# Kernel optimization log

Hardware: AMD Instinct MI355X
Metric: run time of the kernel (lower is better)

## Reference

```python
import jax, jax.numpy as jnp
import numpy as np

HEADS = 16


def setup_inputs() -> dict:
    key = jax.random.key(0)
    ks = jax.random.split(key, 7)
    B, N, MEM, DIM = 2, 2048, 2048, 1024
    J = MEM + N
    x = jax.random.normal(ks[0], (B, N, DIM), dtype=jnp.float32)
    mem = jax.random.normal(ks[1], (B, MEM, DIM), dtype=jnp.float32)
    expire_mask = jax.random.uniform(ks[2], (B, 1, 1, J), dtype=jnp.float32)
    Wq = jax.random.normal(ks[3], (DIM, DIM), dtype=jnp.float32) * 0.02
    Wkv = jax.random.normal(ks[4], (DIM, 2 * DIM), dtype=jnp.float32) * 0.02
    Wo = jax.random.normal(ks[5], (DIM, DIM), dtype=jnp.float32) * 0.02
    bo = jnp.zeros((DIM,), dtype=jnp.float32)
    return {"x": x, "mem": mem, "expire_mask": expire_mask,
            "Wq": Wq, "Wkv": Wkv, "Wo": Wo, "bo": bo}


def reference(x, mem, expire_mask, Wq, Wkv, Wo, bo):
    b, n, dim = x.shape
    h = HEADS
    d = dim // h
    scale = d ** -0.5
    mem_len = mem.shape[1]

    q = x @ Wq                                   # [b, n, dim]
    context = jnp.concatenate([mem, x], axis=1)  # [b, j, dim]
    kv = context @ Wkv                           # [b, j, 2*dim]
    k, v = jnp.split(kv, 2, axis=-1)

    def to_heads(t):
        bb, nn, _ = t.shape
        return t.reshape(bb, nn, h, d).transpose(0, 2, 1, 3)  # b h n d

    q, k, v = map(to_heads, (q, k, v))

    dots = jnp.einsum('bhid,bhjd->bhij', q, k) * scale  # [b,h,n,j]
    j_len = dots.shape[-1]
    # causal mask with memory offset: position i attends to j <= i + mem_len
    i_idx = jnp.arange(n)[:, None]
    j_idx = jnp.arange(j_len)[None, :]
    causal = j_idx > (i_idx + mem_len)           # True => masked
    dots = jnp.where(causal[None, None], -jnp.inf, dots)

    attn = jax.nn.softmax(dots, axis=-1)
    attn = attn * expire_mask                    # post-softmax expire gating

    out = jnp.einsum('bhij,bhjd->bhid', attn, v)  # [b,h,n,d]
    out = out.transpose(0, 2, 1, 3).reshape(b, n, dim)
    return out @ Wo + bo
```

## Files before the change

### kernel.cpp

```cpp
#include <hip/hip_runtime.h>
#include <cstdint>

typedef __bf16 bf16_t;
typedef __attribute__((ext_vector_type(2))) __bf16 bf16x2;
typedef __attribute__((ext_vector_type(4))) __bf16 bf16x4;
typedef __attribute__((ext_vector_type(8))) __bf16 bf16x8;
typedef __attribute__((ext_vector_type(4))) float f32x4;
typedef __attribute__((ext_vector_type(16))) float f32x16;
typedef __attribute__((ext_vector_type(4))) int i32x4;

constexpr int Bx = 2, Nx = 2048, MEMx = 2048, Jx = 4096, DIMx = 1024, Hx = 16, HDx = 64;

__device__ __forceinline__ void gload_lds16(const bf16_t* g, bf16_t* lds) {
  __builtin_amdgcn_global_load_lds(
      (const __attribute__((address_space(1))) unsigned int*)g,
      (__attribute__((address_space(3))) unsigned int*)lds, 16, 0, 0);
}

__device__ __forceinline__ int pk2(float a, float b) {
  bf16x2 t;
  t[0] = (bf16_t)a;
  t[1] = (bf16_t)b;
  return __builtin_bit_cast(int, t);
}

__device__ __forceinline__ void pl32swap(int& a, int& b) {
  asm volatile("v_permlane32_swap_b32 %0, %1" : "+v"(a), "+v"(b));
}

__device__ __forceinline__ float fmax3(float a, float b, float c) {
  float d;
  asm("v_max3_f32 %0, %1, %2, %3" : "=v"(d) : "v"(a), "v"(b), "v"(c));
  return d;
}

__global__ void k_build_bf16(const float* __restrict__ x, const float* __restrict__ mem,
                             bf16_t* __restrict__ xb, bf16_t* __restrict__ ctxb) {
  const int XT = Bx * Nx * DIMx;
  const int CT = Bx * Jx * DIMx;
  for (int i = blockIdx.x * blockDim.x + threadIdx.x; i < XT + CT;
       i += gridDim.x * blockDim.x) {
    if (i < XT) {
      xb[i] = (bf16_t)x[i];
    } else {
      int c = i - XT;
      int bb = c / (Jx * DIMx);
      int rr = c % (Jx * DIMx);
      int j = rr / DIMx, d = rr % DIMx;
      float v = (j < MEMx) ? mem[(int64_t)(bb * MEMx + j) * DIMx + d]
                           : x[(int64_t)(bb * Nx + (j - MEMx)) * DIMx + d];
      ctxb[c] = (bf16_t)v;
    }
  }
}

__global__ void k_transpose_w(const float* __restrict__ W, bf16_t* __restrict__ WT,
                              int K, int Nc) {
  int total = K * Nc;
  for (int i = blockIdx.x * blockDim.x + threadIdx.x; i < total;
       i += gridDim.x * blockDim.x) {
    int n = i / K, k = i % K;
    WT[i] = (bf16_t)W[(int64_t)k * Nc + n];
  }
}

template <int MODE>
__launch_bounds__(256)
__global__ void k_gemm_bt(const bf16_t* __restrict__ A, const bf16_t* __restrict__ BT,
                          void* __restrict__ Cv, const float* __restrict__ bias,
                          const float* __restrict__ gate, bf16_t* __restrict__ VT,
                          float scale, int M, int Nc, int K) {
  __shared__ bf16_t As[2][128 * 32];
  __shared__ bf16_t Bs[2][128 * 32];
  const int tid = threadIdx.x;
  const int w = tid >> 6, l = tid & 63;
  const int lr = l & 15, lg = l >> 4;
  const int m0 = blockIdx.y * 128, n0 = blockIdx.x * 128;
  const int wm = (w >> 1) * 64, wn = (w & 1) * 64;

  const int srow = w * 16 + (l >> 2);
  const int scol = (l & 3) * 8;
  const bf16_t* ga0 = A + (int64_t)(m0 + srow) * K + scol;
  const bf16_t* gb0 = BT + (int64_t)(n0 + srow) * K + scol;

  auto stage = [&](int bufi, int k0) {
    bf16_t* lA = &As[bufi][0] + w * 512;
    bf16_t* lB = &Bs[bufi][0] + w * 512;
    gload_lds16(ga0 + k0, lA);
    gload_lds16(ga0 + (int64_t)64 * K + k0, lA + 2048);
    gload_lds16(gb0 + k0, lB);
    gload_lds16(gb0 + (int64_t)64 * K + k0, lB + 2048);
  };

  f32x4 acc[4][4] = {};

  stage(0, 0);
  __syncthreads();

  const int nsteps = K >> 5;
  for (int t = 0; t < nsteps; ++t) {
    const int cur = t & 1;
    if (t + 1 < nsteps) stage(cur ^ 1, (t + 1) << 5);

    bf16x8 af[4], bfr[4];
#pragma unroll
    for (int q = 0; q < 4; ++q)
      af[q] = *(const bf16x8*)(&As[cur][0] + (wm + q * 16 + lr) * 32 + lg * 8);
#pragma unroll
    for (int q = 0; q < 4; ++q)
      bfr[q] = *(const bf16x8*)(&Bs[cur][0] + (wn + q * 16 + lr) * 32 + lg * 8);
#pragma unroll
    for (int mt = 0; mt < 4; ++mt)
#pragma unroll
      for (int nt = 0; nt < 4; ++nt)
        acc[mt][nt] = __builtin_amdgcn_mfma_f32_16x16x32_bf16(af[mt], bfr[nt],
                                                              acc[mt][nt], 0, 0, 0);
    __syncthreads();
  }

#pragma unroll
  for (int mt = 0; mt < 4; ++mt) {
#pragma unroll
    for (int nt = 0; nt < 4; ++nt) {
      int col = n0 + wn + nt * 16 + lr;
      int row0 = m0 + wm + mt * 16 + lg * 4;
      if constexpr (MODE == 0) {
#pragma unroll
        for (int r = 0; r < 4; ++r)
          ((bf16_t*)Cv)[(int64_t)(row0 + r) * Nc + col] =
              (bf16_t)(acc[mt][nt][r] * scale);
      } else if constexpr (MODE == 1) {
#pragma unroll
        for (int r = 0; r < 4; ++r)
          ((float*)Cv)[(int64_t)(row0 + r) * Nc + col] = acc[mt][nt][r] + bias[col];
      } else {
        if (col < 1024) {
#pragma unroll
          for (int r = 0; r < 4; ++r)
            ((bf16_t*)Cv)[(int64_t)(row0 + r) * 1024 + col] = (bf16_t)acc[mt][nt][r];
        } else {
          int hh = (col - 1024) >> 6, dd = col & 63;
          int bb = row0 >> 12, jj = row0 & (Jx - 1);
          bf16x4 ov;
#pragma unroll
          for (int r = 0; r < 4; ++r)
            ov[r] = (bf16_t)(acc[mt][nt][r] * gate[row0 + r]);
          *(bf16x4*)(VT + (((int64_t)(bb * Hx + hh) * HDx + dd) << 12) + jj) = ov;
        }
      }
    }
  }
}

__launch_bounds__(256)
__global__ void k_attn(const bf16_t* __restrict__ Q, const bf16_t* __restrict__ Kbuf,
                       const bf16_t* __restrict__ VT, bf16_t* __restrict__ Opart,
                       float2* __restrict__ ML) {
  __shared__ bf16_t Ks[2][64 * 64];
  __shared__ bf16_t Vs[2][64 * 64];

  const int tid = threadIdx.x;
  const int w = tid >> 6, l = tid & 63;
  const int ql = l & 31, hi = l >> 5;

  const int lin = blockIdx.x;
  const int qi0 = lin & 15, h = (lin >> 4) & 15;
  const int c = (lin >> 8) & 1, b = lin >> 9;
  const int qi = b ? (15 - qi0) : qi0;
  const int q0 = qi * 128;

  const bf16_t* Qb = Q + ((int64_t)b * Nx) * DIMx + h * HDx;
  const bf16_t* Kb = Kbuf + ((int64_t)b * Jx) * 1024 + h * HDx;
  const bf16_t* Vb = VT + ((int64_t)(b * Hx + h) * HDx << 12);

  const int qrow = q0 + w * 32 + ql;

  bf16x8 qf[4];
#pragma unroll
  for (int dt = 0; dt < 4; ++dt)
    qf[dt] = *(const bf16x8*)(Qb + (int64_t)qrow * DIMx + dt * 16 + hi * 8);
  asm volatile("s_waitcnt vmcnt(0)" ::: "memory");

  int koff[2][4], voff[2][4];
#pragma unroll
  for (int jb = 0; jb < 2; ++jb)
#pragma unroll
    for (int dt = 0; dt < 4; ++dt)
      koff[jb][dt] = (jb * 32 + ql) * 128 + (((dt * 2 + hi) * 16) ^ ((ql & 7) * 16));
#pragma unroll
  for (int db = 0; db < 2; ++db)
#pragma unroll
    for (int jt = 0; jt < 4; ++jt)
      voff[db][jt] = (db * 32 + ql) * 128 + (((jt * 2 + hi) * 16) ^ ((ql & 7) * 16));

  f32x16 o[2] = {};
  float mrun = -1e30f, lsum = 0.f;

  const int srow8 = l >> 3;
  const int swcol = ((l & 7) ^ srow8) * 8;
  const int jstart = c * 2048;
  const int jend = c ? ((Jx < q0 + 128 + MEMx) ? Jx : (q0 + 128 + MEMx)) : 2048;
  const int nt_tiles = (jend - jstart) >> 6;
  const f32x16 z16 = {};

  const bf16_t* ksrc0 = Kb + (int64_t)(w * 16 + srow8) * 1024 + swcol;
  const bf16_t* vsrc0 = Vb + (int64_t)(w * 16 + srow8) * Jx + swcol;

  auto stage = [&](int bufi, int j0) {
    bf16_t* kd = &Ks[bufi][0] + w * 1024;
    const bf16_t* ks = ksrc0 + (int64_t)j0 * 1024;
    gload_lds16(ks, kd);
    gload_lds16(ks + 8 * 1024, kd + 512);
    bf16_t* vd = &Vs[bufi][0] + w * 1024;
    const bf16_t* vs = vsrc0 + j0;
    gload_lds16(vs, vd);
    gload_lds16(vs + 8 * Jx, vd + 512);
  };

  stage(0, jstart);
  stage(1, jstart + 64);

  for (int t = 0; t < nt_tiles; ++t) {
    const int cur = t & 1;
    const int j0 = jstart + (t << 6);
    if (t + 1 < nt_tiles)
      asm volatile("s_waitcnt vmcnt(4)" ::: "memory");
    else
      asm volatile("s_waitcnt vmcnt(0)" ::: "memory");
    __builtin_amdgcn_s_barrier();
    __builtin_amdgcn_sched_barrier(0);

    const char* KsC = (const char*)&Ks[cur][0];
    const char* VsC = (const char*)&Vs[cur][0];

    f32x16 s[2];
    __builtin_amdgcn_s_setprio(1);
#pragma unroll
    for (int jb = 0; jb < 2; ++jb) {
      f32x16 acc = z16;
#pragma unroll
      for (int dt = 0; dt < 4; ++dt) {
        bf16x8 kf = *(const bf16x8*)(KsC + koff[jb][dt]);
        acc = __builtin_amdgcn_mfma_f32_32x32x16_bf16(kf, qf[dt], acc, 0, 0, 0);
      }
      s[jb] = acc;
    }
    __builtin_amdgcn_s_setprio(0);

    if (j0 + 63 > q0 + MEMx) {
#pragma unroll
      for (int jb = 0; jb < 2; ++jb)
#pragma unroll
        for (int r = 0; r < 16; ++r) {
          int j = j0 + jb * 32 + (r & 3) + (r >> 2) * 8 + hi * 4;
          if (j > qrow + MEMx) s[jb][r] = -1e30f;
        }
    }

    float t12[12];
#pragma unroll
    for (int i = 0; i < 10; ++i)
      t12[i] = fmax3(s[(3 * i) >> 4][(3 * i) & 15], s[(3 * i + 1) >> 4][(3 * i + 1) & 15],
                     s[(3 * i + 2) >> 4][(3 * i + 2) & 15]);
    t12[10] = s[1][14];
    t12[11] = s[1][15];
    float t4[4];
#pragma unroll
    for (int i = 0; i < 4; ++i) t4[i] = fmax3(t12[3 * i], t12[3 * i + 1], t12[3 * i + 2]);
    float tm = fmaxf(fmax3(t4[0], t4[1], t4[2]), t4[3]);
    tm = fmaxf(tm, __shfl_xor(tm, 32));

    if (!__all(tm <= mrun + 8.f)) {
      float mnew = fmaxf(mrun, tm);
      float al = exp2f(mrun - mnew);
      mrun = mnew;
      lsum *= al;
#pragma unroll
      for (int db = 0; db < 2; ++db)
#pragma unroll
        for (int r = 0; r < 16; ++r) o[db][r] *= al;
    }

#pragma unroll
    for (int jb = 0; jb < 2; ++jb)
#pragma unroll
      for (int r = 0; r < 16; ++r) s[jb][r] = exp2f(s[jb][r] - mrun);

    f32x16 av = s[0] + s[1];
    float a8[8], a4[4];
#pragma unroll
    for (int i = 0; i < 8; ++i) a8[i] = av[i] + av[i + 8];
#pragma unroll
    for (int i = 0; i < 4; ++i) a4[i] = a8[i] + a8[i + 4];
    float ps = (a4[0] + a4[1]) + (a4[2] + a4[3]);
    ps += __shfl_xor(ps, 32);
    lsum += ps;

    bf16x8 pfrag[4];
#pragma unroll
    for (int jb = 0; jb < 2; ++jb) {
      int pw[8];
#pragma unroll
      for (int g = 0; g < 8; ++g) pw[g] = pk2(s[jb][2 * g], s[jb][2 * g + 1]);
      pl32swap(pw[0], pw[2]);
      pl32swap(pw[1], pw[3]);
      pl32swap(pw[4], pw[6]);
      pl32swap(pw[5], pw[7]);
      i32x4 f0 = {pw[0], pw[1], pw[2], pw[3]};
      i32x4 f1 = {pw[4], pw[5], pw[6], pw[7]};
      pfrag[jb * 2] = __builtin_bit_cast(bf16x8, f0);
      pfrag[jb * 2 + 1] = __builtin_bit_cast(bf16x8, f1);
    }

    __builtin_amdgcn_s_setprio(1);
#pragma unroll
    for (int db = 0; db < 2; ++db)
#pragma unroll
      for (int jt = 0; jt < 4; ++jt) {
        bf16x8 vf = *(const bf16x8*)(VsC + voff[db][jt]);
        o[db] = __builtin_amdgcn_mfma_f32_32x32x16_bf16(vf, pfrag[jt], o[db], 0, 0, 0);
      }
    __builtin_amdgcn_s_setprio(0);

    __builtin_amdgcn_s_barrier();
    __builtin_amdgcn_sched_barrier(0);
    if (t + 2 < nt_tiles) stage(cur, jstart + ((t + 2) << 6));
  }

  bf16_t* op = Opart + (int64_t)c * (Bx * Nx * DIMx) +
               (int64_t)(b * Nx + qrow) * DIMx + h * HDx;
#pragma unroll
  for (int db = 0; db < 2; ++db)
#pragma unroll
    for (int g = 0; g < 4; ++g) {
      bf16x4 ov;
#pragma unroll
      for (int r = 0; r < 4; ++r) ov[r] = (bf16_t)o[db][g * 4 + r];
      *(bf16x4*)(op + db * 32 + g * 8 + hi * 4) = ov;
    }
  if (hi == 0)
    ML[((int64_t)(c * Bx + b) * Hx + h) * Nx + qrow] = make_float2(mrun, lsum);
}

__global__ void k_combine(const bf16_t* __restrict__ Op, const float2* __restrict__ ML,
                          bf16_t* __restrict__ Ho) {
  const int64_t CH = (int64_t)Bx * Nx * DIMx;
  int i = blockIdx.x * blockDim.x + threadIdx.x;
  const int total = (int)(CH >> 3);
  if (i >= total) return;
  int64_t off = (int64_t)i * 8;
  int bqh = (int)(off >> 6);
  int h = bqh & 15;
  int bq = bqh >> 4;
  int b = bq >> 11, q = bq & (Nx - 1);
  float2 ml0 = ML[((int64_t)b * Hx + h) * Nx + q];
  float2 ml1 = ML[((int64_t)(Bx + b) * Hx + h) * Nx + q];
  float M = fmaxf(ml0.x, ml1.x);
  float a0 = exp2f(ml0.x - M), a1 = exp2f(ml1.x - M);
  float inv = 1.f / (a0 * ml0.y + a1 * ml1.y);
  a0 *= inv;
  a1 *= inv;
  bf16x8 v0 = *(const bf16x8*)(Op + off);
  bf16x8 v1 = *(const bf16x8*)(Op + CH + off);
  bf16x8 outv;
#pragma unroll
  for (int r = 0; r < 8; ++r)
    outv[r] = (bf16_t)(a0 * (float)v0[r] + a1 * (float)v1[r]);
  *(bf16x8*)(Ho + off) = outv;
}

extern "C" void kernel_launch(void* const* d_in, const int* in_sizes, int n_in,
                              void* d_out, int out_size, void* d_ws, size_t ws_size,
                              hipStream_t stream) {
  const float* x    = (const float*)d_in[0];
  const float* mem  = (const float*)d_in[1];
  const float* expm = (const float*)d_in[2];
  const float* Wq   = (const float*)d_in[3];
  const float* Wkv  = (const float*)d_in[4];
  const float* Wo   = (const float*)d_in[5];
  const float* bo   = (const float*)d_in[6];
  float* out = (float*)d_out;

  bf16_t* p = (bf16_t*)d_ws;
  bf16_t* xb   = p; p += (size_t)Bx * Nx * DIMx;
  bf16_t* ctxb = p; p += (size_t)Bx * Jx * DIMx;
  bf16_t* WqT  = p; p += (size_t)DIMx * DIMx;
  bf16_t* WkvT = p; p += (size_t)DIMx * 2 * DIMx;
  bf16_t* WoT  = p; p += (size_t)DIMx * DIMx;
  bf16_t* Qb   = p; p += (size_t)Bx * Nx * DIMx;
  bf16_t* KVb  = p; p += (size_t)Bx * Jx * 2 * DIMx;
  bf16_t* Ho   = p; p += (size_t)Bx * Nx * DIMx;

  bf16_t* Kbuf = KVb;
  bf16_t* VT   = KVb + (size_t)Bx * Jx * 1024;
  bf16_t* Opart = ctxb;
  float2* ML    = (float2*)xb;

  k_build_bf16<<<4096, 256, 0, stream>>>(x, mem, xb, ctxb);
  k_transpose_w<<<1024, 256, 0, stream>>>(Wq, WqT, DIMx, DIMx);
  k_transpose_w<<<2048, 256, 0, stream>>>(Wkv, WkvT, DIMx, 2 * DIMx);
  k_transpose_w<<<1024, 256, 0, stream>>>(Wo, WoT, DIMx, DIMx);

  const float qscale = 0.125f * 1.4426950408889634f;
  k_gemm_bt<0><<<dim3(1024 / 128, 4096 / 128), 256, 0, stream>>>(
      xb, WqT, Qb, nullptr, nullptr, nullptr, qscale, Bx * Nx, DIMx, DIMx);
  k_gemm_bt<2><<<dim3(2048 / 128, 8192 / 128), 256, 0, stream>>>(
      ctxb, WkvT, Kbuf, nullptr, expm, VT, 1.0f, Bx * Jx, 2 * DIMx, DIMx);

  k_attn<<<1024, 256, 0, stream>>>(Qb, Kbuf, VT, Opart, ML);
  k_combine<<<(Bx * Nx * DIMx / 8 + 255) / 256, 256, 0, stream>>>(Opart, ML, Ho);

  k_gemm_bt<1><<<dim3(1024 / 128, 4096 / 128), 256, 0, stream>>>(
      Ho, WoT, out, bo, nullptr, nullptr, 1.0f, Bx * Nx, DIMx, DIMx);
}
```

Before: 276.0 us.

## Deepen GEMM prefetch pipeline and compute softmax row sums via MFMA

The projection GEMM now issues two stages of global-to-LDS loads up front and waits with explicit vmcnt counters and raw barriers, so the next tile's loads overlap more of the compute. The attention kernel drops the per-tile VALU reduction and cross-lane shuffle for the softmax denominator. It instead accumulates the row sum with an extra MFMA against a ones vector, and the initial running max becomes 8.0. This adds one MFMA per jt step and uses bf16-rounded probabilities in the sum, and it relies on the vmcnt counts matching the number of outstanding loads.

```diff
diff --git a/kernel.cpp b/kernel.cpp
--- a/kernel.cpp
+++ b/kernel.cpp
@@ -94,13 +94,18 @@
 
   f32x4 acc[4][4] = {};
 
+  const int nsteps = K >> 5;
   stage(0, 0);
-  __syncthreads();
-
-  const int nsteps = K >> 5;
+  stage(1, 32);
+
   for (int t = 0; t < nsteps; ++t) {
     const int cur = t & 1;
-    if (t + 1 < nsteps) stage(cur ^ 1, (t + 1) << 5);
+    if (t + 1 < nsteps)
+      asm volatile("s_waitcnt vmcnt(4)" ::: "memory");
+    else
+      asm volatile("s_waitcnt vmcnt(0)" ::: "memory");
+    __builtin_amdgcn_s_barrier();
+    __builtin_amdgcn_sched_barrier(0);
 
     bf16x8 af[4], bfr[4];
 #pragma unroll
@@ -115,7 +120,9 @@
       for (int nt = 0; nt < 4; ++nt)
         acc[mt][nt] = __builtin_amdgcn_mfma_f32_16x16x32_bf16(af[mt], bfr[nt],
                                                               acc[mt][nt], 0, 0, 0);
-    __syncthreads();
+    __builtin_amdgcn_s_barrier();
+    __builtin_amdgcn_sched_barrier(0);
+    if (t + 2 < nsteps) stage(cur, (t + 2) << 5);
   }
 
 #pragma unroll
@@ -193,8 +200,13 @@
     for (int jt = 0; jt < 4; ++jt)
       voff[db][jt] = (db * 32 + ql) * 128 + (((jt * 2 + hi) * 16) ^ ((ql & 7) * 16));
 
+  bf16x8 onesv;
+#pragma unroll
+  for (int i = 0; i < 8; ++i) onesv[i] = (bf16_t)1.0f;
+
   f32x16 o[2] = {};
-  float mrun = -1e30f, lsum = 0.f;
+  f32x16 ol = {};
+  float mrun = 8.0f;
 
   const int srow8 = l >> 3;
   const int swcol = ((l & 7) ^ srow8) * 8;
@@ -274,7 +286,8 @@
       float mnew = fmaxf(mrun, tm);
       float al = exp2f(mrun - mnew);
       mrun = mnew;
-      lsum *= al;
+#pragma unroll
+      for (int r = 0; r < 16; ++r) ol[r] *= al;
 #pragma unroll
       for (int db = 0; db < 2; ++db)
 #pragma unroll
@@ -285,16 +298,6 @@
     for (int jb = 0; jb < 2; ++jb)
 #pragma unroll
       for (int r = 0; r < 16; ++r) s[jb][r] = exp2f(s[jb][r] - mrun);
-
-    f32x16 av = s[0] + s[1];
-    float a8[8], a4[4];
-#pragma unroll
-    for (int i = 0; i < 8; ++i) a8[i] = av[i] + av[i + 8];
-#pragma unroll
-    for (int i = 0; i < 4; ++i) a4[i] = a8[i] + a8[i + 4];
-    float ps = (a4[0] + a4[1]) + (a4[2] + a4[3]);
-    ps += __shfl_xor(ps, 32);
-    lsum += ps;
 
     bf16x8 pfrag[4];
 #pragma unroll
@@ -314,12 +317,13 @@
 
     __builtin_amdgcn_s_setprio(1);
 #pragma unroll
-    for (int db = 0; db < 2; ++db)
-#pragma unroll
-      for (int jt = 0; jt < 4; ++jt) {
-        bf16x8 vf = *(const bf16x8*)(VsC + voff[db][jt]);
-        o[db] = __builtin_amdgcn_mfma_f32_32x32x16_bf16(vf, pfrag[jt], o[db], 0, 0, 0);
-      }
+    for (int jt = 0; jt < 4; ++jt) {
+      bf16x8 vf0 = *(const bf16x8*)(VsC + voff[0][jt]);
+      o[0] = __builtin_amdgcn_mfma_f32_32x32x16_bf16(vf0, pfrag[jt], o[0], 0, 0, 0);
+      bf16x8 vf1 = *(const bf16x8*)(VsC + voff[1][jt]);
+      o[1] = __builtin_amdgcn_mfma_f32_32x32x16_bf16(vf1, pfrag[jt], o[1], 0, 0, 0);
+      ol = __builtin_amdgcn_mfma_f32_32x32x16_bf16(onesv, pfrag[jt], ol, 0, 0, 0);
+    }
     __builtin_amdgcn_s_setprio(0);
 
     __builtin_amdgcn_s_barrier();
@@ -339,7 +343,7 @@
       *(bf16x4*)(op + db * 32 + g * 8 + hi * 4) = ov;
     }
   if (hi == 0)
-    ML[((int64_t)(c * Bx + b) * Hx + h) * Nx + qrow] = make_float2(mrun, lsum);
+    ML[((int64_t)(c * Bx + b) * Hx + h) * Nx + qrow] = make_float2(mrun, ol[0]);
 }
 
 __global__ void k_combine(const bf16_t* __restrict__ Op, const float2* __restrict__ ML,
```

Result: no change. 270.7 us (-1.9%).
